# Kernel optimization log

Hardware: AMD Instinct MI355X
Metric: run time of the kernel (lower is better)

The kernel has to match this reference:

```python
import jax, jax.numpy as jnp
import numpy as np

B, N, E, H = 8, 2048, 64, 4
D = E * H  # internal width = embedding_dim * num_heads


def _ln(x, g, b):
    m = jnp.mean(x, -1, keepdims=True)
    v = jnp.var(x, -1, keepdims=True)
    return (x - m) / jnp.sqrt(v + 1e-5) * g + b


def setup_inputs() -> dict:
    key = jax.random.key(0)
    ks = jax.random.split(key, 10)

    def lin(k, o, i):
        return jax.random.normal(k, (o, i), jnp.float32) / np.sqrt(i).astype(np.float32)

    return {
        "x": jax.random.normal(ks[0], (B, N, E), jnp.float32),
        "weights": jax.random.uniform(ks[1], (B, N, 1), jnp.float32),
        "ln_g": jnp.ones((E,), jnp.float32),
        "ln_b": jnp.zeros((E,), jnp.float32),
        "wq_w": lin(ks[2], D, E), "wq_b": jnp.zeros((D,), jnp.float32),
        "wk_w": lin(ks[3], D, E), "wk_b": jnp.zeros((D,), jnp.float32),
        "wv_w": lin(ks[4], D, E), "wv_b": jnp.zeros((D,), jnp.float32),
        "mq_w": lin(ks[5], D, D), "mq_b": jnp.zeros((D,), jnp.float32),
        "mk_w": lin(ks[6], D, D), "mk_b": jnp.zeros((D,), jnp.float32),
        "out_w": lin(ks[7], E, D), "out_b": jnp.zeros((E,), jnp.float32),
        "ffn_w": lin(ks[8], E, E), "ffn_b": jnp.zeros((E,), jnp.float32),
    }


def reference(x, weights, ln_g, ln_b, wq_w, wq_b, wk_w, wk_b, wv_w, wv_b,
              mq_w, mq_b, mk_w, mk_b, out_w, out_b, ffn_w, ffn_b):
    Bn, Nn, En = x.shape
    Dd = mq_w.shape[0]
    Hh = Dd // En  # head_dim == embedding_dim in this module

    x_norm = _ln(x, ln_g, ln_b)
    # outer W_q/W_k then nn.MultiheadAttention in-projections (q,k only; v/out_proj are dead)
    q = (x_norm @ wq_w.T + wq_b) @ mq_w.T + mq_b  # [B,N,D]
    k = (x_norm @ wk_w.T + wk_b) @ mk_w.T + mk_b  # [B,N,D]
    q = q.reshape(Bn, Nn, Hh, En)
    k = k.reshape(Bn, Nn, Hh, En)

    scale = np.float32(1.0 / np.sqrt(En))
    scores = jnp.einsum('bihe,bjhe->bhij', q, k) * scale  # [B,H,N,N]
    pad = jnp.sum(weights, -1) == 0.0  # [B,N] key_padding_mask
    scores = jnp.where(pad[:, None, None, :], jnp.float32(-1e9), scores)
    att = jax.nn.softmax(scores, axis=-1).mean(axis=1)  # averaged over heads: [B,N,N]

    # re-weight by input weights and renormalize (second softmax-like pass)
    att = att * weights[..., 0][:, None, :]
    att = att / jnp.sum(att, -1, keepdims=True)

    v = x_norm @ wv_w.T + wv_b  # fresh W_v(x_norm), NOT MHA's value path
    att_out = jnp.einsum('bij,bjd->bid', att, v)  # [B,N,D]

    out1 = x + att_out @ out_w.T + out_b  # [B,N,E]
    out2 = jax.nn.softplus(_ln(out1, ln_g, ln_b) @ ffn_w.T + ffn_b)
    return _ln(out1 + out2, ln_g, ln_b)
```

## Files before the change

### kernel.cpp

```cpp
#include <hip/hip_runtime.h>
#include <hip/hip_bf16.h>

#define BB 8
#define NN 2048
#define EE 64
#define DD 256

typedef __attribute__((ext_vector_type(8))) short short8;
typedef __attribute__((ext_vector_type(4))) float f32x4;
typedef __attribute__((ext_vector_type(4))) unsigned short ushort4v;

#define MFMA16(a, b, c) __builtin_amdgcn_mfma_f32_16x16x32_bf16((a), (b), (c), 0, 0, 0)

__device__ inline void gload16(const void* g, void* l) {
  __builtin_amdgcn_global_load_lds(
      (const __attribute__((address_space(1))) unsigned int*)g,
      (__attribute__((address_space(3))) unsigned int*)l, 16, 0, 0);
}

__device__ inline float bf2f(unsigned short u) {
  union { unsigned int i; float f; } v;
  v.i = ((unsigned int)u) << 16;
  return v.f;
}
__device__ inline unsigned short f2bf(float f) {
  union { float f; unsigned int i; } v;
  v.f = f;
  unsigned int r = v.i + 0x7FFFu + ((v.i >> 16) & 1u);
  return (unsigned short)(r >> 16);
}

__global__ __launch_bounds__(128) void kprep(
    const float* __restrict__ wq_w, const float* __restrict__ wq_b,
    const float* __restrict__ wk_w, const float* __restrict__ wk_b,
    const float* __restrict__ wv_w, const float* __restrict__ mq_w,
    const float* __restrict__ mq_b, const float* __restrict__ mk_w,
    const float* __restrict__ mk_b, const float* __restrict__ out_w,
    const float* __restrict__ ffn_w,
    unsigned short* __restrict__ wqc, float* __restrict__ bqc,
    unsigned short* __restrict__ wkc, float* __restrict__ bkc,
    unsigned short* __restrict__ wvc, unsigned short* __restrict__ outwb,
    unsigned short* __restrict__ ffnwb) {
  const float SC = 0.18033688011112042f;
  int o = blockIdx.x;
  int t = threadIdx.x;
  if (t < 64) {
    float acc = 0.f;
#pragma unroll 4
    for (int d = 0; d < 256; d++) acc += mq_w[o * 256 + d] * wq_w[d * 64 + t];
    wqc[o * 64 + t] = f2bf(acc * SC);
  } else {
    int k = t - 64;
    float acc = 0.f;
#pragma unroll 4
    for (int d = 0; d < 256; d++) acc += mk_w[o * 256 + d] * wk_w[d * 64 + k];
    wkc[o * 64 + k] = f2bf(acc);
  }
  if (t == 0) {
    float acc = 0.f;
    for (int d = 0; d < 256; d++) acc += mq_w[o * 256 + d] * wq_b[d];
    bqc[o] = (acc + mq_b[o]) * SC;
  }
  if (t == 64) {
    float acc = 0.f;
    for (int d = 0; d < 256; d++) acc += mk_w[o * 256 + d] * wk_b[d];
    bkc[o] = acc + mk_b[o];
  }
  int gid = o * 128 + t;
  if (gid < 16384) {
    wvc[gid] = f2bf(wv_w[gid]);
    outwb[gid] = f2bf(out_w[gid]);
  }
  if (gid < 4096) ffnwb[gid] = f2bf(ffn_w[gid]);
}

__global__ __launch_bounds__(128, 2) void kproj(
    const float* __restrict__ x, const float* __restrict__ ln_g,
    const float* __restrict__ ln_b, const unsigned short* __restrict__ wqc,
    const float* __restrict__ bqc, const unsigned short* __restrict__ wkc,
    const float* __restrict__ bkc, const unsigned short* __restrict__ wvc,
    const float* __restrict__ wv_b, unsigned short* __restrict__ qout,
    unsigned short* __restrict__ kout, unsigned short* __restrict__ vtout) {
  __shared__ __align__(1024) char lds[2 * 10240];
  int tid = threadIdx.x;
  int w = tid >> 6, l = tid & 63;
  int c = l & 15, g = l >> 4;
  int blk = blockIdx.x;
  int b = blk >> 6;
  int i0 = (blk & 63) * 32 + w * 16;
  size_t row0 = (size_t)b * NN + i0;
  char* xnb = lds + w * 10240;
  char* tlb = lds + w * 10240 + 2048;

  int rl = l >> 2;
  int cc = (l & 3) * 16;
  float xv[16];
  {
    const float* xr = x + (row0 + rl) * EE + cc;
#pragma unroll
    for (int i = 0; i < 4; i++) {
      float4 v = *(const float4*)(xr + i * 4);
      xv[i * 4 + 0] = v.x; xv[i * 4 + 1] = v.y;
      xv[i * 4 + 2] = v.z; xv[i * 4 + 3] = v.w;
    }
  }
  float s = 0.f, s2 = 0.f;
#pragma unroll
  for (int i = 0; i < 16; i++) { s += xv[i]; s2 += xv[i] * xv[i]; }
  s += __shfl_xor(s, 1); s += __shfl_xor(s, 2);
  s2 += __shfl_xor(s2, 1); s2 += __shfl_xor(s2, 2);
  float mean = s * (1.f / 64.f);
  float var = s2 * (1.f / 64.f) - mean * mean;
  float rstd = rsqrtf(var + 1e-5f);
  {
    int swzr = (rl & 7) << 4;
    unsigned short pk[16];
#pragma unroll
    for (int i = 0; i < 16; i++)
      pk[i] = f2bf((xv[i] - mean) * rstd * ln_g[cc + i] + ln_b[cc + i]);
#pragma unroll
    for (int hh = 0; hh < 2; hh++) {
      short8 d;
#pragma unroll
      for (int i = 0; i < 8; i++) d[i] = (short)pk[hh * 8 + i];
      *(short8*)(xnb + rl * 128 + (((l & 3) * 32 + hh * 16) ^ swzr)) = d;
    }
  }
  __syncthreads();

  int swz = (c & 7) << 4;
  int o2_0 = (g * 16) ^ swz;
  int o2_1 = (64 + g * 16) ^ swz;
  short8 af0 = *(const short8*)(xnb + c * 128 + o2_0);
  short8 af1 = *(const short8*)(xnb + c * 128 + o2_1);

#pragma unroll
  for (int dt = 0; dt < 16; dt++) {
    float bias = bqc[dt * 16 + c];
    f32x4 acc = {bias, bias, bias, bias};
    acc = MFMA16(af0, *(const short8*)(wqc + (dt * 16 + c) * 64 + g * 8), acc);
    acc = MFMA16(af1, *(const short8*)(wqc + (dt * 16 + c) * 64 + 32 + g * 8), acc);
#pragma unroll
    for (int r = 0; r < 4; r++) {
      int row = 4 * g + r;
      *(unsigned short*)(tlb + row * 512 + ((dt * 32 + 2 * c) ^ ((row & 7) << 4))) = f2bf(acc[r]);
    }
  }
  __syncthreads();
#pragma unroll
  for (int c2 = 0; c2 < 8; c2++) {
    int flat = c2 * 1024 + l * 16;
    int rowt = flat >> 9;
    int off = flat & 511;
    short8 d = *(const short8*)(tlb + rowt * 512 + (off ^ ((rowt & 7) << 4)));
    *(short8*)((char*)qout + (row0 + rowt) * 512 + off) = d;
  }
  __syncthreads();

#pragma unroll
  for (int dt = 0; dt < 16; dt++) {
    float bias = bkc[dt * 16 + c];
    f32x4 acc = {bias, bias, bias, bias};
    acc = MFMA16(af0, *(const short8*)(wkc + (dt * 16 + c) * 64 + g * 8), acc);
    acc = MFMA16(af1, *(const short8*)(wkc + (dt * 16 + c) * 64 + 32 + g * 8), acc);
#pragma unroll
    for (int r = 0; r < 4; r++) {
      int row = 4 * g + r;
      *(unsigned short*)(tlb + row * 512 + ((dt * 32 + 2 * c) ^ ((row & 7) << 4))) = f2bf(acc[r]);
    }
  }
  __syncthreads();
#pragma unroll
  for (int c2 = 0; c2 < 8; c2++) {
    int flat = c2 * 1024 + l * 16;
    int rowt = flat >> 9;
    int off = flat & 511;
    short8 d = *(const short8*)(tlb + rowt * 512 + (off ^ ((rowt & 7) << 4)));
    *(short8*)((char*)kout + (row0 + rowt) * 512 + off) = d;
  }

#pragma unroll
  for (int dt = 0; dt < 16; dt++) {
    float bias = wv_b[dt * 16 + c];
    f32x4 acc = {bias, bias, bias, bias};
    acc = MFMA16(af0, *(const short8*)(wvc + (dt * 16 + c) * 64 + g * 8), acc);
    acc = MFMA16(af1, *(const short8*)(wvc + (dt * 16 + c) * 64 + 32 + g * 8), acc);
    ushort4v pk;
#pragma unroll
    for (int r = 0; r < 4; r++) pk[r] = f2bf(acc[r]);
    *(ushort4v*)(vtout + ((size_t)b * 256 + dt * 16 + c) * NN + i0 + 4 * g) = pk;
  }
}

__global__ __launch_bounds__(256, 2) void kpass1(
    const unsigned short* __restrict__ qb, const unsigned short* __restrict__ kb,
    const float* __restrict__ wts, float* __restrict__ lout) {
  __shared__ __align__(1024) char ldsk[16384];
  int tid = threadIdx.x;
  int w = tid >> 6, l = tid & 63, c = l & 15, g = l >> 4;
  int p = blockIdx.x;
  int q = (p & 7) * 64 + (p >> 3);
  int y = q >> 8, b = (q >> 5) & 7, it = q & 31;
  int i0 = it * 64 + w * 16;
  short8 qf[8];
  {
    const unsigned short* qr = qb + ((size_t)b * NN + i0 + c) * DD;
#pragma unroll
    for (int s = 0; s < 8; s++) qf[s] = *(const short8*)(qr + s * 32 + g * 8);
  }
  float ls[16];
#pragma unroll
  for (int i = 0; i < 16; i++) ls[i] = 0.f;
  int swz = (c & 7) << 4;
  int o2_0 = (g * 16) ^ swz;
  int o2_1 = (64 + g * 16) ^ swz;
  const char* kb0 = ldsk + c * 512;

  for (int jt = 0; jt < 32; jt++) {
    int jb = y * 1024 + jt * 32;
    __syncthreads();
#pragma unroll
    for (int call = 0; call < 4; call++) {
      int chunk = call * 256 + tid;
      int j = chunk >> 5;
      int q16 = (chunk & 31) << 4;
      const char* src = (const char*)(kb + ((size_t)b * NN + jb + j) * DD) + (q16 ^ ((j & 7) << 4));
      gload16(src, ldsk + (chunk & ~63) * 16);
    }
    __syncthreads();
    float wm[2];
#pragma unroll
    for (int js = 0; js < 2; js++) {
      float wv = wts[(size_t)b * NN + jb + js * 16 + c];
      wm[js] = (wv == 0.f) ? 0.f : 1.f;
    }
#pragma unroll
    for (int h = 0; h < 4; h++) {
#pragma unroll
      for (int js = 0; js < 2; js++) {
        f32x4 s4 = {0.f, 0.f, 0.f, 0.f};
        s4 = MFMA16(qf[2 * h], *(const short8*)(kb0 + js * 8192 + h * 128 + o2_0), s4);
        s4 = MFMA16(qf[2 * h + 1], *(const short8*)(kb0 + js * 8192 + h * 128 + o2_1), s4);
#pragma unroll
        for (int r = 0; r < 4; r++) ls[h * 4 + r] += exp2f(s4[r]) * wm[js];
      }
    }
  }
#pragma unroll
  for (int xm = 1; xm <= 8; xm <<= 1)
#pragma unroll
    for (int i = 0; i < 16; i++) ls[i] += __shfl_xor(ls[i], xm);
  if (c == 0) {
#pragma unroll
    for (int h = 0; h < 4; h++)
#pragma unroll
      for (int r = 0; r < 4; r++)
        lout[(((size_t)y * BB + b) * 4 + h) * NN + i0 + 4 * g + r] = ls[h * 4 + r];
  }
}

__global__ __launch_bounds__(256, 2) void kpass2(
    const unsigned short* __restrict__ qb, const unsigned short* __restrict__ kb,
    const unsigned short* __restrict__ vt, const float* __restrict__ wts,
    const float* __restrict__ lin_, unsigned short* __restrict__ num,
    float* __restrict__ tout) {
  __shared__ __align__(1024) char lds[16384 + 16384 + 4 * 1280];
  int tid = threadIdx.x;
  int w = tid >> 6, l = tid & 63, c = l & 15, g = l >> 4;
  char* ldsk = lds;
  char* ldsv = lds + 16384;
  char* ldsp = lds + 32768 + w * 1280;
  int p = blockIdx.x;
  int q = (p & 7) * 64 + (p >> 3);
  int y = q >> 8, b = (q >> 5) & 7, it = q & 31;
  int i0 = it * 64 + w * 16;

  float nl[16];
#pragma unroll
  for (int h = 0; h < 4; h++)
#pragma unroll
    for (int r = 0; r < 4; r++) {
      size_t ia = (((size_t)0 * BB + b) * 4 + h) * NN + i0 + 4 * g + r;
      size_t ib = (((size_t)1 * BB + b) * 4 + h) * NN + i0 + 4 * g + r;
      nl[h * 4 + r] = -log2f(lin_[ia] + lin_[ib]);
    }

  short8 qf[8];
  {
    const unsigned short* qr = qb + ((size_t)b * NN + i0 + c) * DD;
#pragma unroll
    for (int s = 0; s < 8; s++) qf[s] = *(const short8*)(qr + s * 32 + g * 8);
  }
  f32x4 acc[16];
#pragma unroll
  for (int i = 0; i < 16; i++) acc[i] = (f32x4){0.f, 0.f, 0.f, 0.f};
  float tacc[4] = {0.f, 0.f, 0.f, 0.f};
  int swz = (c & 7) << 4;
  int o2_0 = (g * 16) ^ swz;
  int o2_1 = (64 + g * 16) ^ swz;
  const char* kb0 = ldsk + c * 512;
  const char* vb0 = ldsv + c * 16;
  int pw[8];
#pragma unroll
  for (int js = 0; js < 2; js++)
#pragma unroll
    for (int r = 0; r < 4; r++) pw[js * 4 + r] = (4 * g + r) * 80 + js * 32 + 2 * c;
  const char* prd = ldsp + c * 80 + g * 16;

  for (int jt = 0; jt < 32; jt++) {
    int jb = y * 1024 + jt * 32;
    __syncthreads();
#pragma unroll
    for (int call = 0; call < 4; call++) {
      int chunk = call * 256 + tid;
      int j = chunk >> 5;
      int q16 = (chunk & 31) << 4;
      const char* src = (const char*)(kb + ((size_t)b * NN + jb + j) * DD) + (q16 ^ ((j & 7) << 4));
      gload16(src, ldsk + (chunk & ~63) * 16);
    }
#pragma unroll
    for (int call = 0; call < 4; call++) {
      int i = call * 256 + tid;
      int cc = i & 15, joct = (i >> 4) & 3, dt2 = i >> 6;
      int d = dt2 * 16 + cc;
      const char* src = (const char*)(vt + ((size_t)b * 256 + d) * NN + jb + joct * 8);
      gload16(src, ldsv + (i & ~63) * 16);
    }
    __syncthreads();
    float wj[2];
#pragma unroll
    for (int js = 0; js < 2; js++) wj[js] = wts[(size_t)b * NN + jb + js * 16 + c];
    float av[2][4];
#pragma unroll
    for (int js = 0; js < 2; js++) {
#pragma unroll
      for (int r = 0; r < 4; r++) av[js][r] = 0.f;
#pragma unroll
      for (int h = 0; h < 4; h++) {
        f32x4 s4 = {nl[h * 4 + 0], nl[h * 4 + 1], nl[h * 4 + 2], nl[h * 4 + 3]};
        s4 = MFMA16(qf[2 * h], *(const short8*)(kb0 + js * 8192 + h * 128 + o2_0), s4);
        s4 = MFMA16(qf[2 * h + 1], *(const short8*)(kb0 + js * 8192 + h * 128 + o2_1), s4);
#pragma unroll
        for (int r = 0; r < 4; r++) av[js][r] += exp2f(s4[r]);
      }
#pragma unroll
      for (int r = 0; r < 4; r++) { av[js][r] *= wj[js]; tacc[r] += av[js][r]; }
    }
#pragma unroll
    for (int js = 0; js < 2; js++)
#pragma unroll
      for (int r = 0; r < 4; r++)
        *(unsigned short*)(ldsp + pw[js * 4 + r]) = f2bf(av[js][r]);
    asm volatile("s_waitcnt lgkmcnt(0)" ::: "memory");
    __builtin_amdgcn_sched_barrier(0);
    short8 pf = *(const short8*)prd;
#pragma unroll
    for (int dt = 0; dt < 16; dt++) {
      short8 vf = *(const short8*)(vb0 + dt * 1024 + g * 256);
      acc[dt] = MFMA16(pf, vf, acc[dt]);
    }
  }
#pragma unroll
  for (int xm = 1; xm <= 8; xm <<= 1)
#pragma unroll
    for (int r = 0; r < 4; r++) tacc[r] += __shfl_xor(tacc[r], xm);
#pragma unroll
  for (int dt = 0; dt < 16; dt++)
#pragma unroll
    for (int r = 0; r < 4; r++)
      num[(((size_t)y * BB + b) * NN + i0 + 4 * g + r) * DD + dt * 16 + c] = f2bf(acc[dt][r]);
  if (c == 0)
#pragma unroll
    for (int r = 0; r < 4; r++)
      tout[((size_t)y * BB + b) * NN + i0 + 4 * g + r] = tacc[r];
}

__global__ __launch_bounds__(128, 2) void kfinal(
    const unsigned short* __restrict__ num, const float* __restrict__ tws,
    const float* __restrict__ x, const unsigned short* __restrict__ outwb,
    const float* __restrict__ out_b, const float* __restrict__ ln_g,
    const float* __restrict__ ln_b, const unsigned short* __restrict__ ffnwb,
    const float* __restrict__ ffn_b, float* __restrict__ out) {
  __shared__ __align__(1024) char lds[2 * 2304];
  int tid = threadIdx.x, w = tid >> 6, l = tid & 63, c = l & 15, g = l >> 4;
  int blk = blockIdx.x;
  int b = blk >> 6;
  int i0 = (blk & 63) * 32 + w * 16;
  char* hb = lds + w * 2304;

  short8 af[8];
  {
    const unsigned short* p0 = num + (((size_t)0 * BB + b) * NN + i0 + c) * DD;
    const unsigned short* p1 = num + (((size_t)1 * BB + b) * NN + i0 + c) * DD;
#pragma unroll
    for (int s = 0; s < 8; s++) {
      short8 a0 = *(const short8*)(p0 + s * 32 + g * 8);
      short8 a1 = *(const short8*)(p1 + s * 32 + g * 8);
      short8 o;
#pragma unroll
      for (int t2 = 0; t2 < 8; t2++)
        o[t2] = (short)f2bf(bf2f((unsigned short)a0[t2]) + bf2f((unsigned short)a1[t2]));
      af[s] = o;
    }
  }
  float trow[4];
#pragma unroll
  for (int r = 0; r < 4; r++)
    trow[r] = tws[((size_t)0 * BB + b) * NN + i0 + 4 * g + r] +
              tws[((size_t)1 * BB + b) * NN + i0 + 4 * g + r];
  f32x4 acc[4];
#pragma unroll
  for (int ct = 0; ct < 4; ct++) {
    acc[ct] = (f32x4){0.f, 0.f, 0.f, 0.f};
#pragma unroll
    for (int s = 0; s < 8; s++)
      acc[ct] = MFMA16(af[s], *(const short8*)(outwb + (ct * 16 + c) * DD + s * 32 + g * 8), acc[ct]);
  }
  float gv[4], bvv[4], obv[4], fbv[4];
#pragma unroll
  for (int ct = 0; ct < 4; ct++) {
    gv[ct] = ln_g[ct * 16 + c]; bvv[ct] = ln_b[ct * 16 + c];
    obv[ct] = out_b[ct * 16 + c]; fbv[ct] = ffn_b[ct * 16 + c];
  }
  float o1[4][4];
#pragma unroll
  for (int ct = 0; ct < 4; ct++)
#pragma unroll
    for (int r = 0; r < 4; r++)
      o1[ct][r] = x[((size_t)b * NN + i0 + 4 * g + r) * EE + ct * 16 + c] +
                  acc[ct][r] / trow[r] + obv[ct];
  float h1[4][4];
#pragma unroll
  for (int r = 0; r < 4; r++) {
    float s = o1[0][r] + o1[1][r] + o1[2][r] + o1[3][r];
    float s2 = o1[0][r] * o1[0][r] + o1[1][r] * o1[1][r] +
               o1[2][r] * o1[2][r] + o1[3][r] * o1[3][r];
#pragma unroll
    for (int xm = 1; xm < 16; xm <<= 1) { s += __shfl_xor(s, xm); s2 += __shfl_xor(s2, xm); }
    float mean = s * (1.f / 64.f);
    float var = s2 * (1.f / 64.f) - mean * mean;
    float rstd = rsqrtf(var + 1e-5f);
#pragma unroll
    for (int ct = 0; ct < 4; ct++)
      h1[ct][r] = (o1[ct][r] - mean) * rstd * gv[ct] + bvv[ct];
  }
#pragma unroll
  for (int ct = 0; ct < 4; ct++)
#pragma unroll
    for (int r = 0; r < 4; r++)
      *(unsigned short*)(hb + (4 * g + r) * 144 + ct * 32 + 2 * c) = f2bf(h1[ct][r]);
  asm volatile("s_waitcnt lgkmcnt(0)" ::: "memory");
  __builtin_amdgcn_sched_barrier(0);
  short8 hf0 = *(const short8*)(hb + c * 144 + g * 16);
  short8 hf1 = *(const short8*)(hb + c * 144 + 64 + g * 16);
  f32x4 a2[4];
#pragma unroll
  for (int ct = 0; ct < 4; ct++) {
    a2[ct] = (f32x4){0.f, 0.f, 0.f, 0.f};
    a2[ct] = MFMA16(hf0, *(const short8*)(ffnwb + (ct * 16 + c) * EE + g * 8), a2[ct]);
    a2[ct] = MFMA16(hf1, *(const short8*)(ffnwb + (ct * 16 + c) * EE + 32 + g * 8), a2[ct]);
  }
  float o3[4][4];
#pragma unroll
  for (int ct = 0; ct < 4; ct++)
#pragma unroll
    for (int r = 0; r < 4; r++) {
      float vv = a2[ct][r] + fbv[ct];
      float sp = fmaxf(vv, 0.f) + log1pf(expf(-fabsf(vv)));
      o3[ct][r] = o1[ct][r] + sp;
    }
#pragma unroll
  for (int r = 0; r < 4; r++) {
    float s = o3[0][r] + o3[1][r] + o3[2][r] + o3[3][r];
    float s2 = o3[0][r] * o3[0][r] + o3[1][r] * o3[1][r] +
               o3[2][r] * o3[2][r] + o3[3][r] * o3[3][r];
#pragma unroll
    for (int xm = 1; xm < 16; xm <<= 1) { s += __shfl_xor(s, xm); s2 += __shfl_xor(s2, xm); }
    float mean = s * (1.f / 64.f);
    float var = s2 * (1.f / 64.f) - mean * mean;
    float rstd = rsqrtf(var + 1e-5f);
#pragma unroll
    for (int ct = 0; ct < 4; ct++)
      out[((size_t)b * NN + i0 + 4 * g + r) * EE + ct * 16 + c] =
          (o3[ct][r] - mean) * rstd * gv[ct] + bvv[ct];
  }
}

extern "C" void kernel_launch(void* const* d_in, const int* in_sizes, int n_in,
                              void* d_out, int out_size, void* d_ws, size_t ws_size,
                              hipStream_t stream) {
  (void)in_sizes; (void)n_in; (void)out_size; (void)ws_size;
  const float* x = (const float*)d_in[0];
  const float* wts = (const float*)d_in[1];
  const float* ln_g = (const float*)d_in[2];
  const float* ln_b = (const float*)d_in[3];
  const float* wq_w = (const float*)d_in[4];
  const float* wq_b = (const float*)d_in[5];
  const float* wk_w = (const float*)d_in[6];
  const float* wk_b = (const float*)d_in[7];
  const float* wv_w = (const float*)d_in[8];
  const float* wv_b = (const float*)d_in[9];
  const float* mq_w = (const float*)d_in[10];
  const float* mq_b = (const float*)d_in[11];
  const float* mk_w = (const float*)d_in[12];
  const float* mk_b = (const float*)d_in[13];
  const float* out_w = (const float*)d_in[14];
  const float* out_b = (const float*)d_in[15];
  const float* ffn_w = (const float*)d_in[16];
  const float* ffn_b = (const float*)d_in[17];
  float* out = (float*)d_out;

  char* ws = (char*)d_ws;
  unsigned short* qb = (unsigned short*)(ws + 0);
  unsigned short* kb = (unsigned short*)(ws + 8388608);
  unsigned short* vt = (unsigned short*)(ws + 16777216);
  float* l1 = (float*)(ws + 25165824);
  unsigned short* num = (unsigned short*)(ws + 26214400);
  float* tws = (float*)(ws + 42991616);
  unsigned short* wqc = (unsigned short*)(ws + 43122688);
  unsigned short* wkc = (unsigned short*)(ws + 43155456);
  unsigned short* wvc = (unsigned short*)(ws + 43188224);
  float* bqc = (float*)(ws + 43220992);
  float* bkc = (float*)(ws + 43222016);
  unsigned short* outwb = (unsigned short*)(ws + 43223040);
  unsigned short* ffnwb = (unsigned short*)(ws + 43255808);

  kprep<<<256, 128, 0, stream>>>(wq_w, wq_b, wk_w, wk_b, wv_w, mq_w, mq_b,
                                 mk_w, mk_b, out_w, ffn_w, wqc, bqc, wkc, bkc,
                                 wvc, outwb, ffnwb);
  kproj<<<512, 128, 0, stream>>>(x, ln_g, ln_b, wqc, bqc, wkc, bkc, wvc, wv_b,
                                 qb, kb, vt);
  kpass1<<<512, 256, 0, stream>>>(qb, kb, wts, l1);
  kpass2<<<512, 256, 0, stream>>>(qb, kb, vt, wts, l1, num, tws);
  kfinal<<<512, 128, 0, stream>>>(num, tws, x, outwb, out_b, ln_g, ln_b, ffnwb,
                                  ffn_b, out);
}
```

Before: 277.5 us.

## Double-buffer K/V LDS tiles to overlap global loads with MFMA compute

Both attention passes now keep two LDS buffers. The next key (and value) tile is fetched with global_load_lds while the current tile is being consumed, so each iteration needs one barrier instead of two and load latency can hide behind compute. kpass1 also doubles its key tile to 64 rows, which halves its loop trip count. The cost is much more LDS per block (about 64–70 KB), which could limit occupancy, and the compiler's vmcnt wait still lands at the barrier.

New measurement: 269.4 us. 2.9% less time.

```diff
diff --git a/kernel.cpp b/kernel.cpp
--- a/kernel.cpp
+++ b/kernel.cpp
@@ -195,7 +195,7 @@
 __global__ __launch_bounds__(256, 2) void kpass1(
     const unsigned short* __restrict__ qb, const unsigned short* __restrict__ kb,
     const float* __restrict__ wts, float* __restrict__ lout) {
-  __shared__ __align__(1024) char ldsk[16384];
+  __shared__ __align__(1024) char ldsk[2 * 32768];
   int tid = threadIdx.x;
   int w = tid >> 6, l = tid & 63, c = l & 15, g = l >> 4;
   int p = blockIdx.x;
@@ -214,30 +214,46 @@
   int swz = (c & 7) << 4;
   int o2_0 = (g * 16) ^ swz;
   int o2_1 = (64 + g * 16) ^ swz;
-  const char* kb0 = ldsk + c * 512;
-
-  for (int jt = 0; jt < 32; jt++) {
-    int jb = y * 1024 + jt * 32;
-    __syncthreads();
-#pragma unroll
-    for (int call = 0; call < 4; call++) {
+  const size_t brow = (size_t)b * NN;
+
+  {
+    int jb = y * 1024;
+#pragma unroll
+    for (int call = 0; call < 8; call++) {
       int chunk = call * 256 + tid;
       int j = chunk >> 5;
       int q16 = (chunk & 31) << 4;
-      const char* src = (const char*)(kb + ((size_t)b * NN + jb + j) * DD) + (q16 ^ ((j & 7) << 4));
+      const char* src = (const char*)(kb + (brow + jb + j) * DD) + (q16 ^ ((j & 7) << 4));
       gload16(src, ldsk + (chunk & ~63) * 16);
     }
+  }
+  for (int jt = 0; jt < 16; jt++) {
+    int jb = y * 1024 + jt * 64;
+    const char* kcur = ldsk + (jt & 1) * 32768;
+    char* knxt = ldsk + ((jt + 1) & 1) * 32768;
     __syncthreads();
-    float wm[2];
-#pragma unroll
-    for (int js = 0; js < 2; js++) {
-      float wv = wts[(size_t)b * NN + jb + js * 16 + c];
+    if (jt < 15) {
+      int jb2 = jb + 64;
+#pragma unroll
+      for (int call = 0; call < 8; call++) {
+        int chunk = call * 256 + tid;
+        int j = chunk >> 5;
+        int q16 = (chunk & 31) << 4;
+        const char* src = (const char*)(kb + (brow + jb2 + j) * DD) + (q16 ^ ((j & 7) << 4));
+        gload16(src, knxt + (chunk & ~63) * 16);
+      }
+    }
+    float wm[4];
+#pragma unroll
+    for (int js = 0; js < 4; js++) {
+      float wv = wts[brow + jb + js * 16 + c];
       wm[js] = (wv == 0.f) ? 0.f : 1.f;
     }
+    const char* kb0 = kcur + c * 512;
 #pragma unroll
     for (int h = 0; h < 4; h++) {
 #pragma unroll
-      for (int js = 0; js < 2; js++) {
+      for (int js = 0; js < 4; js++) {
         f32x4 s4 = {0.f, 0.f, 0.f, 0.f};
         s4 = MFMA16(qf[2 * h], *(const short8*)(kb0 + js * 8192 + h * 128 + o2_0), s4);
         s4 = MFMA16(qf[2 * h + 1], *(const short8*)(kb0 + js * 8192 + h * 128 + o2_1), s4);
@@ -264,16 +280,17 @@
     const unsigned short* __restrict__ vt, const float* __restrict__ wts,
     const float* __restrict__ lin_, unsigned short* __restrict__ num,
     float* __restrict__ tout) {
-  __shared__ __align__(1024) char lds[16384 + 16384 + 4 * 1280];
+  __shared__ __align__(1024) char lds[2 * 16384 + 2 * 16384 + 4 * 1280];
   int tid = threadIdx.x;
   int w = tid >> 6, l = tid & 63, c = l & 15, g = l >> 4;
   char* ldsk = lds;
-  char* ldsv = lds + 16384;
-  char* ldsp = lds + 32768 + w * 1280;
+  char* ldsv = lds + 32768;
+  char* ldsp = lds + 65536 + w * 1280;
   int p = blockIdx.x;
   int q = (p & 7) * 64 + (p >> 3);
   int y = q >> 8, b = (q >> 5) & 7, it = q & 31;
   int i0 = it * 64 + w * 16;
+  const size_t brow = (size_t)b * NN;
 
   float nl[16];
 #pragma unroll
@@ -287,7 +304,7 @@
 
   short8 qf[8];
   {
-    const unsigned short* qr = qb + ((size_t)b * NN + i0 + c) * DD;
+    const unsigned short* qr = qb + (brow + i0 + c) * DD;
 #pragma unroll
     for (int s = 0; s < 8; s++) qf[s] = *(const short8*)(qr + s * 32 + g * 8);
   }
@@ -298,8 +315,6 @@
   int swz = (c & 7) << 4;
   int o2_0 = (g * 16) ^ swz;
   int o2_1 = (64 + g * 16) ^ swz;
-  const char* kb0 = ldsk + c * 512;
-  const char* vb0 = ldsv + c * 16;
   int pw[8];
 #pragma unroll
   for (int js = 0; js < 2; js++)
@@ -307,29 +322,55 @@
     for (int r = 0; r < 4; r++) pw[js * 4 + r] = (4 * g + r) * 80 + js * 32 + 2 * c;
   const char* prd = ldsp + c * 80 + g * 16;
 
-  for (int jt = 0; jt < 32; jt++) {
-    int jb = y * 1024 + jt * 32;
-    __syncthreads();
+  {
+    int jb = y * 1024;
 #pragma unroll
     for (int call = 0; call < 4; call++) {
       int chunk = call * 256 + tid;
       int j = chunk >> 5;
       int q16 = (chunk & 31) << 4;
-      const char* src = (const char*)(kb + ((size_t)b * NN + jb + j) * DD) + (q16 ^ ((j & 7) << 4));
+      const char* src = (const char*)(kb + (brow + jb + j) * DD) + (q16 ^ ((j & 7) << 4));
       gload16(src, ldsk + (chunk & ~63) * 16);
     }
 #pragma unroll
     for (int call = 0; call < 4; call++) {
       int i = call * 256 + tid;
       int cc = i & 15, joct = (i >> 4) & 3, dt2 = i >> 6;
-      int d = dt2 * 16 + cc;
-      const char* src = (const char*)(vt + ((size_t)b * 256 + d) * NN + jb + joct * 8);
+      const char* src = (const char*)(vt + ((size_t)b * 256 + dt2 * 16 + cc) * NN + jb + joct * 8);
       gload16(src, ldsv + (i & ~63) * 16);
     }
+  }
+
+  for (int jt = 0; jt < 32; jt++) {
+    int jb = y * 1024 + jt * 32;
+    const char* kcur = ldsk + (jt & 1) * 16384;
+    const char* vcur = ldsv + (jt & 1) * 16384;
+    char* knxt = ldsk + ((jt + 1) & 1) * 16384;
+    char* vnxt = ldsv + ((jt + 1) & 1) * 16384;
     __syncthreads();
+    if (jt < 31) {
+      int jb2 = jb + 32;
+#pragma unroll
+      for (int call = 0; call < 4; call++) {
+        int chunk = call * 256 + tid;
+        int j = chunk >> 5;
+        int q16 = (chunk & 31) << 4;
+        const char* src = (const char*)(kb + (brow + jb2 + j) * DD) + (q16 ^ ((j & 7) << 4));
+        gload16(src, knxt + (chunk & ~63) * 16);
+      }
+#pragma unroll
+      for (int call = 0; call < 4; call++) {
+        int i = call * 256 + tid;
+        int cc = i & 15, joct = (i >> 4) & 3, dt2 = i >> 6;
+        const char* src = (const char*)(vt + ((size_t)b * 256 + dt2 * 16 + cc) * NN + jb2 + joct * 8);
+        gload16(src, vnxt + (i & ~63) * 16);
+      }
+    }
     float wj[2];
 #pragma unroll
-    for (int js = 0; js < 2; js++) wj[js] = wts[(size_t)b * NN + jb + js * 16 + c];
+    for (int js = 0; js < 2; js++) wj[js] = wts[brow + jb + js * 16 + c];
+    const char* kb0 = kcur + c * 512;
+    const char* vb0 = vcur + c * 16;
     float av[2][4];
 #pragma unroll
     for (int js = 0; js < 2; js++) {
```
